# Optimization experiments

Measured on AMD Instinct MI355X. Metric: run time of the kernel, lower is better.

## Reference

```python
import jax, jax.numpy as jnp
import numpy as np

B, M = 512, 256
IN1, IN2, IN3 = 20000, 15000, 20000


def setup_inputs() -> dict:
    key = jax.random.key(0)
    ks = jax.random.split(key, 16)
    s1, s2, s3, s4 = 1.0 / np.sqrt(IN1), 1.0 / np.sqrt(IN2), 1.0 / np.sqrt(IN3), 1.0 / np.sqrt(4 * M)
    return {
        "expression": jax.random.normal(ks[0], (B, IN1), jnp.float32),
        "mutation": jax.random.uniform(ks[1], (B, IN2), jnp.float32),
        "cna": jax.random.normal(ks[2], (B, IN3), jnp.float32),
        "We_x": jax.random.normal(ks[3], (M, IN1), jnp.float32) * s1,
        "We_y": jax.random.normal(ks[4], (M, IN1), jnp.float32) * s1,
        "Wm_x": jax.random.normal(ks[5], (M, IN2), jnp.float32) * s2,
        "Wm_y": jax.random.normal(ks[6], (M, IN2), jnp.float32) * s2,
        "Wc_x": jax.random.normal(ks[7], (M, IN3), jnp.float32) * s3,
        "Wc_y": jax.random.normal(ks[8], (M, IN3), jnp.float32) * s3,
        "W3e": jax.random.normal(ks[9], (1, 4 * M), jnp.float32) * s4,
        "b3e": jnp.zeros((1,), jnp.float32),
        "W3m": jax.random.normal(ks[10], (1, 4 * M), jnp.float32) * s4,
        "b3m": jnp.zeros((1,), jnp.float32),
        "W3c": jax.random.normal(ks[11], (1, 4 * M), jnp.float32) * s4,
        "b3c": jnp.zeros((1,), jnp.float32),
    }


def reference(expression, mutation, cna, We_x, We_y, Wm_x, Wm_y, Wc_x, Wc_y,
              W3e, b3e, W3m, b3m, W3c, b3c):
    def proj(x, Wx, Wy):  # (B,F) -> (B,2,M)
        return jnp.stack([x @ Wx.T, x @ Wy.T], axis=1)

    def l2norm(t):  # normalize over the 2-row axis, like torch.norm(dim=1,keepdim=True)
        return t / jnp.linalg.norm(t, axis=1, keepdims=True)

    e = l2norm(proj(expression, We_x, We_y))
    m = l2norm(proj(mutation, Wm_x, Wm_y))
    c = l2norm(proj(cna, Wc_x, Wc_y))

    energy = lambda a, b: jnp.einsum('bkm,bkn->bmn', a, b)  # (B,M,M), k=2
    E_em, E_ec, E_mc = energy(e, m), energy(e, c), energy(m, c)

    att_em = jax.nn.softmax(E_em, axis=1)                     # softmax over dim1
    att_ec = jax.nn.softmax(E_ec, axis=1)
    att_me = jnp.swapaxes(jax.nn.softmax(E_em, axis=-1), 1, 2)
    att_mc = jax.nn.softmax(E_mc, axis=-1)                    # double permute cancels
    att_ce = jnp.swapaxes(jax.nn.softmax(E_ec, axis=-1), 1, 2)
    att_cm = jnp.swapaxes(jax.nn.softmax(E_mc, axis=-1), 1, 2)

    w = lambda x, a: jnp.einsum('bkm,bmn->bkn', x, a)  # (B,2,M)
    e_feat = jnp.concatenate([w(e, att_em), w(e, att_ec)], axis=1).reshape(-1, 4 * e.shape[-1])
    m_feat = jnp.concatenate([w(m, att_me), w(m, att_mc)], axis=1).reshape(-1, 4 * e.shape[-1])
    c_feat = jnp.concatenate([w(c, att_ce), w(c, att_cm)], axis=1).reshape(-1, 4 * e.shape[-1])

    head = lambda f, W, b: jnp.squeeze(jax.nn.sigmoid(f @ W.T + b))
    return head(e_feat, W3e, b3e), head(m_feat, W3m, b3m), head(c_feat, W3c, b3c)
```

## Files before the change

kernel.cpp:

```cpp
#include <hip/hip_runtime.h>
#include <hip/hip_bf16.h>

typedef short short8 __attribute__((ext_vector_type(8)));
typedef float float4v __attribute__((ext_vector_type(4)));

#define TK 32
#define MAXSPLIT 16
#define APAD 40

typedef const __attribute__((address_space(1))) void* gas_ptr;
typedef __attribute__((address_space(3))) void* las_ptr;

__device__ __forceinline__ void dma16(const float* g, float* l) {
    __builtin_amdgcn_global_load_lds((gas_ptr)g, (las_ptr)l, 16, 0, 0);
}

__device__ __forceinline__ unsigned int bfrne(float f) {
    unsigned int u = __builtin_bit_cast(unsigned int, f);
    return (u + 0x7fffu + ((u >> 16) & 1u)) >> 16;
}
__device__ __forceinline__ unsigned int pack2bf(float a, float b) {
    return bfrne(a) | (bfrne(b) << 16);
}

__global__ __launch_bounds__(256, 3) void gemm_kernel(
    const float* __restrict__ Ae, const float* __restrict__ Am, const float* __restrict__ Ac,
    const float* __restrict__ Wex, const float* __restrict__ Wey,
    const float* __restrict__ Wmx, const float* __restrict__ Wmy,
    const float* __restrict__ Wcx, const float* __restrict__ Wcy,
    float* __restrict__ part, int nsplit)
{
    int nb = gridDim.x;
    int per = nb >> 3;
    int bid = blockIdx.x;
    int job = (bid & 7) * per + (bid >> 3);

    int mod = job / (16 * nsplit);
    int rem = job - mod * 16 * nsplit;
    int split = rem >> 4;
    int t2 = rem & 15;
    int ti = t2 >> 2, tj = t2 & 3;

    const float* A; const float* Wx; const float* Wy; int K;
    if (mod == 0)      { A = Ae; Wx = Wex; Wy = Wey; K = 20000; }
    else if (mod == 1) { A = Am; Wx = Wmx; Wy = Wmy; K = 15000; }
    else               { A = Ac; Wx = Wcx; Wy = Wcy; K = 20000; }

    int chunk = ((K + nsplit * TK - 1) / (nsplit * TK)) * TK;
    int kstart = split * chunk;
    int kend = kstart + chunk; if (kend > K) kend = K;
    int nstep = (kend - kstart + TK - 1) / TK;

    const float* Abase = A + (size_t)(ti * 128) * K;
    const float* Wbase = (tj < 2) ? (Wx + (size_t)(tj * 128) * K)
                                  : (Wy + (size_t)((tj - 2) * 128) * K);

    __shared__ unsigned short As[2][128][APAD];
    __shared__ float Bs[2][128 * 32];

    int tid = threadIdx.x;
    int lane = tid & 63, w = tid >> 6;
    int wr = (w >> 1) * 64, wc = (w & 1) * 64;
    int q = lane >> 4, r16 = lane & 15, q8 = q * 8;

    int ra0 = tid >> 3;
    int ca  = (tid & 7) * 4;
    int lrow = lane >> 3, l8 = lane & 7;

    float4v ar[4];
    auto loadA = [&](int k0) {
        int k = k0 + ca; if (k > K - 4) k = K - 4;
        #pragma unroll
        for (int i = 0; i < 4; ++i)
            ar[i] = *(const float4v*)(Abase + (size_t)(ra0 + i * 32) * K + k);
    };
    auto storeA = [&](int buf, int k0, bool tail) {
        bool kill = tail && (k0 + ca >= kend);
        #pragma unroll
        for (int i = 0; i < 4; ++i) {
            float4v v = ar[i];
            if (kill) v = (float4v){0.f, 0.f, 0.f, 0.f};
            uint2 pk;
            pk.x = pack2bf(v[0], v[1]);
            pk.y = pack2bf(v[2], v[3]);
            *(uint2*)&As[buf][ra0 + i * 32][ca] = pk;
        }
    };
    auto dmaB = [&](int buf, int k0) {
        float* base = &Bs[buf][0];
        #pragma unroll
        for (int i = 0; i < 4; ++i) {
            int c = i * 4 + w;
            int r = c * 8 + lrow;
            int g = l8 ^ (r & 7);
            int k = k0 + g * 4; if (k > K - 4) k = K - 4;
            dma16(Wbase + (size_t)r * K + k, base + c * 256);
        }
    };

    float4v acc[4][4];
    #pragma unroll
    for (int a = 0; a < 4; ++a)
        #pragma unroll
        for (int b = 0; b < 4; ++b)
            acc[a][b] = (float4v){0.f, 0.f, 0.f, 0.f};

    auto computeStep = [&](int buf, int k0, bool tail) {
        short8 fa[4], fb[4];
        #pragma unroll
        for (int a = 0; a < 4; ++a)
            fa[a] = *(const short8*)&As[buf][wr + a * 16 + r16][q8];
        #pragma unroll
        for (int b = 0; b < 4; ++b) {
            int r = wc + b * 16 + r16;
            int rx = r & 7;
            const float* rowp = &Bs[buf][r * 32];
            float4v g0 = *(const float4v*)(rowp + (((2 * q)     ^ rx) * 4));
            float4v g1 = *(const float4v*)(rowp + (((2 * q + 1) ^ rx) * 4));
            if (tail) {
                if (k0 + q8 >= kend)     g0 = (float4v){0.f, 0.f, 0.f, 0.f};
                if (k0 + q8 + 4 >= kend) g1 = (float4v){0.f, 0.f, 0.f, 0.f};
            }
            union { unsigned int u[4]; short8 s; } pk;
            pk.u[0] = pack2bf(g0[0], g0[1]);
            pk.u[1] = pack2bf(g0[2], g0[3]);
            pk.u[2] = pack2bf(g1[0], g1[1]);
            pk.u[3] = pack2bf(g1[2], g1[3]);
            fb[b] = pk.s;
        }
        #pragma unroll
        for (int a = 0; a < 4; ++a)
            #pragma unroll
            for (int b = 0; b < 4; ++b)
                acc[a][b] = __builtin_amdgcn_mfma_f32_16x16x32_bf16(fa[a], fb[b], acc[a][b], 0, 0, 0);
    };

    loadA(kstart);
    dmaB(0, kstart);
    storeA(0, kstart, kstart + TK > kend);

    for (int s = 0; s < nstep; ++s) {
        int cur = s & 1;
        int k0 = kstart + s * TK;
        int k1 = k0 + TK;
        bool more = (s + 1 < nstep);
        __syncthreads();
        if (more) { dmaB(cur ^ 1, k1); loadA(k1); }
        computeStep(cur, k0, k1 > kend);
        if (more) storeA(cur ^ 1, k1, k1 + TK > kend);
    }

    float* pbase = part + (size_t)((mod * 16 + t2) * nsplit + split) * 16384;
    #pragma unroll
    for (int a = 0; a < 4; ++a)
        #pragma unroll
        for (int b = 0; b < 4; ++b)
            #pragma unroll
            for (int r = 0; r < 4; ++r) {
                int row = wr + a * 16 + (lane >> 4) * 4 + r;
                int col = wc + b * 16 + r16;
                pbase[row * 128 + col] = acc[a][b][r];
            }
}

__global__ void reduce_kernel(const float* __restrict__ part, float* __restrict__ P,
                              float* __restrict__ headacc, int nsplit)
{
    int gid = blockIdx.x * 256 + threadIdx.x;
    if (gid < 1536) headacc[gid] = 0.f;
    int mod = gid >> 18;
    int rem = gid & 262143;
    int b = rem >> 9, j = rem & 511;
    int ti = b >> 7, r = b & 127, tj = j >> 7, c = j & 127;
    int t2 = ti * 4 + tj;
    const float* src = part + (size_t)((mod * 16 + t2) * nsplit) * 16384 + r * 128 + c;
    float s = 0.f;
    for (int k = 0; k < nsplit; ++k) s += src[(size_t)k * 16384];
    P[gid] = s;
}

__global__ __launch_bounds__(256) void pairs_kernel(
    const float* __restrict__ P, float* __restrict__ headacc,
    const float* __restrict__ W3e, const float* __restrict__ W3m, const float* __restrict__ W3c)
{
    int b = blockIdx.x / 3, pair = blockIdx.x % 3;
    int t = threadIdx.x;
    __shared__ float2 Pn[256], Qn[256];
    __shared__ float Rinv[256];
    __shared__ float red[4];

    int pm = (pair == 2) ? 1 : 0;
    int qm = (pair == 0) ? 1 : 2;
    const float* prow = P + pm * 262144 + b * 512;
    const float* qrow = P + qm * 262144 + b * 512;

    float px = prow[t], py = prow[256 + t];
    float ip = rsqrtf(px * px + py * py);
    Pn[t] = (float2){px * ip, py * ip};
    float qx = qrow[t], qy = qrow[256 + t];
    float iq = rsqrtf(qx * qx + qy * qy);
    Qn[t] = (float2){qx * iq, qy * iq};
    __syncthreads();

    const float L2E = 1.4426950408889634f;

    float pxr = Pn[t].x * L2E, pyr = Pn[t].y * L2E;
    float rs = 0.f, rqx = 0.f, rqy = 0.f;
    #pragma unroll 4
    for (int j = 0; j < 256; ++j) {
        float2 qv = Qn[j];
        float x = exp2f(fmaf(pyr, qv.y, pxr * qv.x));
        rs += x;
        rqx = fmaf(qv.x, x, rqx);
        rqy = fmaf(qv.y, x, rqy);
    }
    float rinv = 1.f / rs;
    Rinv[t] = rinv;
    float Fq0 = rqx * rinv, Fq1 = rqy * rinv;

    const float* WR; int hR, offR;
    if (pair == 0)      { WR = W3m; hR = 1; offR = 0; }
    else if (pair == 1) { WR = W3c; hR = 2; offR = 0; }
    else                { WR = W3c; hR = 2; offR = 512; }
    float v = Fq0 * WR[offR + t] + Fq1 * WR[offR + 256 + t];
    #pragma unroll
    for (int o = 32; o > 0; o >>= 1) v += __shfl_down(v, o, 64);
    if ((t & 63) == 0) red[t >> 6] = v;
    __syncthreads();
    if (t == 0) atomicAdd(&headacc[b * 3 + hR], red[0] + red[1] + red[2] + red[3]);
    __syncthreads();

    float qxr = Qn[t].x * L2E, qyr = Qn[t].y * L2E;
    float cs = 0.f, cpx = 0.f, cpy = 0.f;
    if (pair < 2) {
        #pragma unroll 4
        for (int i = 0; i < 256; ++i) {
            float2 pv = Pn[i];
            float x = exp2f(fmaf(qyr, pv.y, qxr * pv.x));
            cs += x;
            cpx = fmaf(pv.x, x, cpx);
            cpy = fmaf(pv.y, x, cpy);
        }
        float ci = 1.f / cs;
        cpx *= ci; cpy *= ci;
    } else {
        #pragma unroll 4
        for (int i = 0; i < 256; ++i) {
            float2 pv = Pn[i];
            float x = exp2f(fmaf(qyr, pv.y, qxr * pv.x)) * Rinv[i];
            cpx = fmaf(pv.x, x, cpx);
            cpy = fmaf(pv.y, x, cpy);
        }
    }
    const float* WC; int hC, offC;
    if (pair == 0)      { WC = W3e; hC = 0; offC = 0; }
    else if (pair == 1) { WC = W3e; hC = 0; offC = 512; }
    else                { WC = W3m; hC = 1; offC = 512; }
    float v2 = cpx * WC[offC + t] + cpy * WC[offC + 256 + t];
    #pragma unroll
    for (int o = 32; o > 0; o >>= 1) v2 += __shfl_down(v2, o, 64);
    if ((t & 63) == 0) red[t >> 6] = v2;
    __syncthreads();
    if (t == 0) atomicAdd(&headacc[b * 3 + hC], red[0] + red[1] + red[2] + red[3]);
}

__global__ void head_kernel(const float* __restrict__ headacc,
                            const float* __restrict__ b3e, const float* __restrict__ b3m,
                            const float* __restrict__ b3c, float* __restrict__ out)
{
    int i = blockIdx.x * 256 + threadIdx.x;
    if (i >= 1536) return;
    int h = i >> 9, b = i & 511;
    float bias = (h == 0) ? b3e[0] : (h == 1) ? b3m[0] : b3c[0];
    float z = headacc[b * 3 + h] + bias;
    out[i] = 1.f / (1.f + __expf(-z));
}

extern "C" void kernel_launch(void* const* d_in, const int* in_sizes, int n_in,
                              void* d_out, int out_size, void* d_ws, size_t ws_size,
                              hipStream_t stream) {
    const float* Ae  = (const float*)d_in[0];
    const float* Am  = (const float*)d_in[1];
    const float* Ac  = (const float*)d_in[2];
    const float* Wex = (const float*)d_in[3];
    const float* Wey = (const float*)d_in[4];
    const float* Wmx = (const float*)d_in[5];
    const float* Wmy = (const float*)d_in[6];
    const float* Wcx = (const float*)d_in[7];
    const float* Wcy = (const float*)d_in[8];
    const float* W3e = (const float*)d_in[9];
    const float* b3e = (const float*)d_in[10];
    const float* W3m = (const float*)d_in[11];
    const float* b3m = (const float*)d_in[12];
    const float* W3c = (const float*)d_in[13];
    const float* b3c = (const float*)d_in[14];

    size_t fixed = (size_t)786432 * 4 + 1536 * 4;
    int nsplit = 2;
    if (ws_size > fixed) {
        size_t avail = (ws_size - fixed) / ((size_t)48 * 16384 * 4);
        nsplit = (avail < MAXSPLIT) ? (int)avail : MAXSPLIT;
        if (nsplit < 1) nsplit = 1;
    }

    float* part    = (float*)d_ws;
    float* P       = part + (size_t)48 * nsplit * 16384;
    float* headacc = P + 786432;

    gemm_kernel<<<48 * nsplit, 256, 0, stream>>>(Ae, Am, Ac, Wex, Wey, Wmx, Wmy, Wcx, Wcy,
                                                 part, nsplit);
    reduce_kernel<<<3072, 256, 0, stream>>>(part, P, headacc, nsplit);
    pairs_kernel<<<1536, 256, 0, stream>>>(P, headacc, W3e, W3m, W3c);
    head_kernel<<<6, 256, 0, stream>>>(headacc, b3e, b3m, b3c, (float*)d_out);
}
```

Before: 354.4 us.

## Stage W tiles as bf16 via registers instead of fp32 LDS DMA

The W operand was previously DMA'd into LDS as fp32 with a swizzle, and every wave converted it to bf16 in the compute loop. It now goes through registers like A and is converted once to bf16 before the LDS store. This removes repeated per-wave conversion and halves the LDS footprint for B. Bf16 packing also switches to the hardware v_cvt_pk_bf16_f32 instruction. In exchange the asynchronous DMA path is lost, so register pressure rises with 8 float4 prefetch registers per thread.

```diff
diff --git a/kernel.cpp b/kernel.cpp
--- a/kernel.cpp
+++ b/kernel.cpp
@@ -8,19 +8,10 @@
 #define MAXSPLIT 16
 #define APAD 40
 
-typedef const __attribute__((address_space(1))) void* gas_ptr;
-typedef __attribute__((address_space(3))) void* las_ptr;
-
-__device__ __forceinline__ void dma16(const float* g, float* l) {
-    __builtin_amdgcn_global_load_lds((gas_ptr)g, (las_ptr)l, 16, 0, 0);
-}
-
-__device__ __forceinline__ unsigned int bfrne(float f) {
-    unsigned int u = __builtin_bit_cast(unsigned int, f);
-    return (u + 0x7fffu + ((u >> 16) & 1u)) >> 16;
-}
 __device__ __forceinline__ unsigned int pack2bf(float a, float b) {
-    return bfrne(a) | (bfrne(b) << 16);
+    unsigned int r;
+    asm("v_cvt_pk_bf16_f32 %0, %1, %2" : "=v"(r) : "v"(a), "v"(b));
+    return r;
 }
 
 __global__ __launch_bounds__(256, 3) void gemm_kernel(
@@ -56,7 +47,7 @@
                                   : (Wy + (size_t)((tj - 2) * 128) * K);
 
     __shared__ unsigned short As[2][128][APAD];
-    __shared__ float Bs[2][128 * 32];
+    __shared__ unsigned short Bs[2][128][APAD];
 
     int tid = threadIdx.x;
     int lane = tid & 63, w = tid >> 6;
@@ -65,36 +56,29 @@
 
     int ra0 = tid >> 3;
     int ca  = (tid & 7) * 4;
-    int lrow = lane >> 3, l8 = lane & 7;
-
-    float4v ar[4];
-    auto loadA = [&](int k0) {
+
+    float4v ar[4], br[4];
+    auto loadAB = [&](int k0) {
         int k = k0 + ca; if (k > K - 4) k = K - 4;
         #pragma unroll
-        for (int i = 0; i < 4; ++i)
+        for (int i = 0; i < 4; ++i) {
             ar[i] = *(const float4v*)(Abase + (size_t)(ra0 + i * 32) * K + k);
+            br[i] = *(const float4v*)(Wbase + (size_t)(ra0 + i * 32) * K + k);
+        }
     };
-    auto storeA = [&](int buf, int k0, bool tail) {
+    auto storeAB = [&](int buf, int k0, bool tail) {
         bool kill = tail && (k0 + ca >= kend);
         #pragma unroll
         for (int i = 0; i < 4; ++i) {
-            float4v v = ar[i];
-            if (kill) v = (float4v){0.f, 0.f, 0.f, 0.f};
-            uint2 pk;
-            pk.x = pack2bf(v[0], v[1]);
-            pk.y = pack2bf(v[2], v[3]);
-            *(uint2*)&As[buf][ra0 + i * 32][ca] = pk;
-        }
-    };
-    auto dmaB = [&](int buf, int k0) {
-        float* base = &Bs[buf][0];
-        #pragma unroll
-        for (int i = 0; i < 4; ++i) {
-            int c = i * 4 + w;
-            int r = c * 8 + lrow;
-            int g = l8 ^ (r & 7);
-            int k = k0 + g * 4; if (k > K - 4) k = K - 4;
-            dma16(Wbase + (size_t)r * K + k, base + c * 256);
+            float4v va = ar[i], vb = br[i];
+            if (kill) { va = (float4v){0.f,0.f,0.f,0.f}; vb = (float4v){0.f,0.f,0.f,0.f}; }
+            uint2 pa, pb;
+            pa.x = pack2bf(va[0], va[1]);
+            pa.y = pack2bf(va[2], va[3]);
+            pb.x = pack2bf(vb[0], vb[1]);
+            pb.y = pack2bf(vb[2], vb[3]);
+            *(uint2*)&As[buf][ra0 + i * 32][ca] = pa;
+            *(uint2*)&Bs[buf][ra0 + i * 32][ca] = pb;
         }
     };
 
@@ -105,29 +89,14 @@
         for (int b = 0; b < 4; ++b)
             acc[a][b] = (float4v){0.f, 0.f, 0.f, 0.f};
 
-    auto computeStep = [&](int buf, int k0, bool tail) {
+    auto computeStep = [&](int buf) {
         short8 fa[4], fb[4];
         #pragma unroll
         for (int a = 0; a < 4; ++a)
             fa[a] = *(const short8*)&As[buf][wr + a * 16 + r16][q8];
         #pragma unroll
-        for (int b = 0; b < 4; ++b) {
-            int r = wc + b * 16 + r16;
-            int rx = r & 7;
-            const float* rowp = &Bs[buf][r * 32];
-            float4v g0 = *(const float4v*)(rowp + (((2 * q)     ^ rx) * 4));
-            float4v g1 = *(const float4v*)(rowp + (((2 * q + 1) ^ rx) * 4));
-            if (tail) {
-                if (k0 + q8 >= kend)     g0 = (float4v){0.f, 0.f, 0.f, 0.f};
-                if (k0 + q8 + 4 >= kend) g1 = (float4v){0.f, 0.f, 0.f, 0.f};
-            }
-            union { unsigned int u[4]; short8 s; } pk;
-            pk.u[0] = pack2bf(g0[0], g0[1]);
-            pk.u[1] = pack2bf(g0[2], g0[3]);
-            pk.u[2] = pack2bf(g1[0], g1[1]);
-            pk.u[3] = pack2bf(g1[2], g1[3]);
-            fb[b] = pk.s;
-        }
+        for (int b = 0; b < 4; ++b)
+            fb[b] = *(const short8*)&Bs[buf][wc + b * 16 + r16][q8];
         #pragma unroll
         for (int a = 0; a < 4; ++a)
             #pragma unroll
@@ -135,19 +104,17 @@
                 acc[a][b] = __builtin_amdgcn_mfma_f32_16x16x32_bf16(fa[a], fb[b], acc[a][b], 0, 0, 0);
     };
 
-    loadA(kstart);
-    dmaB(0, kstart);
-    storeA(0, kstart, kstart + TK > kend);
+    loadAB(kstart);
+    storeAB(0, kstart, kstart + TK > kend);
 
     for (int s = 0; s < nstep; ++s) {
         int cur = s & 1;
-        int k0 = kstart + s * TK;
-        int k1 = k0 + TK;
+        int k1 = kstart + (s + 1) * TK;
         bool more = (s + 1 < nstep);
         __syncthreads();
-        if (more) { dmaB(cur ^ 1, k1); loadA(k1); }
-        computeStep(cur, k0, k1 > kend);
-        if (more) storeA(cur ^ 1, k1, k1 + TK > kend);
+        if (more) loadAB(k1);
+        computeStep(cur);
+        if (more) storeAB(cur ^ 1, k1, k1 + TK > kend);
     }
 
     float* pbase = part + (size_t)((mod * 16 + t2) * nsplit + split) * 16384;
```

After: 353.8 us. No clear change (-0.2%).
